# Optimization experiments

Hardware: AMD Instinct MI355X
Metric: run time of the kernel (lower is better)

## Reference

```python
import jax, jax.numpy as jnp
import numpy as np

# Static configuration (matches init_kwargs)
EMBED_DIM = 256
NUM_HEADS = 8
NUM_LEVELS = 4
NUM_POINTS = 16
N_DEGREE = 3
HEAD_DIM = EMBED_DIM // NUM_HEADS
SPATIAL_SHAPES = ((64, 64), (32, 32), (16, 16), (8, 8))  # (H, W) per level
LEN_V = sum(h * w for h, w in SPATIAL_SHAPES)


def _bilinear_gather(v, loc, Hl, Wl):
    """Bilinear sampling with zero padding, align_corners=False.
    v:   [bs, nH, Hl*Wl, hd]  flattened level feature map (per head)
    loc: [bs, nH, Q, 2]       (x, y) in [0, 1]
    returns [bs, nH, Q, hd]
    """
    x = loc[..., 0] * Wl - 0.5
    y = loc[..., 1] * Hl - 0.5
    x0 = jnp.floor(x)
    y0 = jnp.floor(y)
    wx = x - x0
    wy = y - y0
    out = jnp.zeros(v.shape[:2] + (loc.shape[2], v.shape[-1]), v.dtype)
    corners = ((0, 0, (1 - wx) * (1 - wy)), (1, 0, wx * (1 - wy)),
               (0, 1, (1 - wx) * wy), (1, 1, wx * wy))
    for dx, dy, w in corners:
        xi = x0 + dx
        yi = y0 + dy
        valid = (xi >= 0) & (xi < Wl) & (yi >= 0) & (yi < Hl)
        idx = (jnp.clip(yi, 0, Hl - 1) * Wl + jnp.clip(xi, 0, Wl - 1)).astype(jnp.int32)
        g = jnp.take_along_axis(v, idx[..., None], axis=2)  # [bs,nH,Q,hd]
        out = out + g * (w * valid.astype(w.dtype))[..., None]
    return out


def setup_inputs() -> dict:
    key = jax.random.key(0)
    ks = jax.random.split(key, 12)
    bs, Lq = 4, 1024
    s = 0.02
    return {
        "query": jax.random.normal(ks[0], (bs, Lq, EMBED_DIM), jnp.float32),
        # polynomial coefficients for x(l), y(l); scaled so curves stay roughly in [0,1]
        "reference_points": jax.random.uniform(ks[1], (bs, Lq, 2 * (N_DEGREE + 1)), jnp.float32) * 0.25,
        "value": jax.random.normal(ks[2], (bs, LEN_V, EMBED_DIM), jnp.float32),
        "W_value": jax.random.normal(ks[3], (EMBED_DIM, EMBED_DIM), jnp.float32) * s,
        "b_value": jnp.zeros((EMBED_DIM,), jnp.float32),
        "W_offsets": jax.random.normal(ks[4], (EMBED_DIM, NUM_HEADS * NUM_LEVELS * NUM_POINTS * 2), jnp.float32) * s,
        "b_offsets": jax.random.normal(ks[5], (NUM_HEADS * NUM_LEVELS * NUM_POINTS * 2,), jnp.float32) * 0.5,
        "W_attn": jax.random.normal(ks[6], (EMBED_DIM, NUM_HEADS * NUM_LEVELS * NUM_POINTS), jnp.float32) * s,
        "b_attn": jnp.zeros((NUM_HEADS * NUM_LEVELS * NUM_POINTS,), jnp.float32),
        "W_out": jax.random.normal(ks[7], (EMBED_DIM, EMBED_DIM), jnp.float32) * s,
        "b_out": jnp.zeros((EMBED_DIM,), jnp.float32),
    }


def reference(query, reference_points, value, W_value, b_value, W_offsets,
              b_offsets, W_attn, b_attn, W_out, b_out):
    bs, Lq, _ = query.shape
    Lv = value.shape[1]
    nH, nL, nP, hd = NUM_HEADS, NUM_LEVELS, NUM_POINTS, HEAD_DIM

    v = (value @ W_value + b_value).reshape(bs, Lv, nH, hd)

    sampling_offsets = (query @ W_offsets + b_offsets).reshape(bs, Lq, nH, nL, nP, 2)
    attn = jax.nn.softmax((query @ W_attn + b_attn).reshape(bs, Lq, nH, nL * nP), axis=-1)
    attn = attn.reshape(bs, Lq, nH, nL, nP)

    # reference_points last dim == 8: polynomial branch
    lambdaz = jnp.linspace(0.0, 1.0, nP)
    lambdas = jnp.stack([lambdaz ** i for i in range(N_DEGREE, -1, -1)], axis=1)  # [nP, deg+1]
    ref_polys = reference_points.reshape(bs, Lq, 2, N_DEGREE + 1)
    pnts = jnp.einsum('bqcd,pd->bqpc', ref_polys, lambdas)  # [bs,Lq,nP,2] (x,y)

    # offset_normalizer: spatial shapes flipped -> (W, H) per level
    normalizer = jnp.array([[w, h] for (h, w) in SPATIAL_SHAPES], jnp.float32)
    normalizer = normalizer.reshape(1, 1, 1, nL, 1, 2)
    sampling_locations = pnts[:, :, None, None, :, :] + sampling_offsets / normalizer
    # -> [bs, Lq, nH, nL, nP, 2] in [0,1]

    # deformable attention core: per-level bilinear gather + softmax-weighted sum
    out = jnp.zeros((bs, Lq, nH, hd), v.dtype)
    start = 0
    for lvl, (Hl, Wl) in enumerate(SPATIAL_SHAPES):
        v_l = v[:, start:start + Hl * Wl].transpose(0, 2, 1, 3)  # [bs,nH,Hl*Wl,hd]
        loc_l = sampling_locations[:, :, :, lvl]                 # [bs,Lq,nH,nP,2]
        loc_l = loc_l.transpose(0, 2, 1, 3, 4).reshape(bs, nH, Lq * nP, 2)
        sampled = _bilinear_gather(v_l, loc_l, Hl, Wl).reshape(bs, nH, Lq, nP, hd)
        out = out + jnp.einsum('bhqpd,bqhp->bqhd', sampled, attn[:, :, :, lvl])
        start += Hl * Wl

    output = out.reshape(bs, Lq, nH * hd) @ W_out + b_out
    return output, sampling_locations, attn
```

## Files before the change

### kernel.cpp

```cpp
#include <hip/hip_runtime.h>
#include <math.h>

#define BS 4
#define LQ 1024
#define EMB 256
#define NH 8
#define NL 4
#define NP 16
#define HD 32
#define LV 5440
#define KDIM 256

typedef __attribute__((ext_vector_type(8))) short short8;
typedef __attribute__((ext_vector_type(4))) float f32x4;

__device__ inline unsigned short f2bf(float f) {
    unsigned u = __builtin_bit_cast(unsigned, f);
    u += 0x7fff + ((u >> 16) & 1);
    return (unsigned short)(u >> 16);
}

__global__ __launch_bounds__(256) void prep(const float* __restrict__ Wv,
                                            const float* __restrict__ Wo,
                                            const float* __restrict__ Wa,
                                            const float* __restrict__ Wu,
                                            const float* __restrict__ value,
                                            const float* __restrict__ query,
                                            unsigned short* __restrict__ Wt,
                                            unsigned short* __restrict__ val_bf,
                                            unsigned short* __restrict__ qry_bf) {
    const int blk = blockIdx.x;
    if (blk < 512) {
        __shared__ float tile[32][33];
        const int n0 = (blk & 63) * 32, k0 = (blk >> 6) * 32;
        const float* src; int N, nloc;
        if (n0 < 256)       { src = Wv; N = 256;  nloc = n0; }
        else if (n0 < 1280) { src = Wo; N = 1024; nloc = n0 - 256; }
        else if (n0 < 1792) { src = Wa; N = 512;  nloc = n0 - 1280; }
        else                { src = Wu; N = 256;  nloc = n0 - 1792; }
        const int tx = threadIdx.x & 31, ty = threadIdx.x >> 5;
#pragma unroll
        for (int i = 0; i < 32; i += 8)
            tile[ty + i][tx] = src[(size_t)(k0 + ty + i) * N + nloc + tx];
        __syncthreads();
#pragma unroll
        for (int i = 0; i < 32; i += 8)
            Wt[(size_t)(n0 + ty + i) * KDIM + k0 + tx] = f2bf(tile[tx][ty + i]);
    } else {
        const int i = (blk - 512) * 256 + threadIdx.x;
        const float* src;
        unsigned short* dst;
        size_t off;
        if (i < 696320) { src = value; dst = val_bf; off = (size_t)i * 8; }
        else            { src = query; dst = qry_bf; off = (size_t)(i - 696320) * 8; }
        const float4 f0 = *(const float4*)(src + off);
        const float4 f1 = *(const float4*)(src + off + 4);
        short8 h;
        h[0] = (short)f2bf(f0.x); h[1] = (short)f2bf(f0.y);
        h[2] = (short)f2bf(f0.z); h[3] = (short)f2bf(f0.w);
        h[4] = (short)f2bf(f1.x); h[5] = (short)f2bf(f1.y);
        h[6] = (short)f2bf(f1.z); h[7] = (short)f2bf(f1.w);
        *(short8*)(dst + off) = h;
    }
}

template <int MODE>
__device__ __forceinline__ void gemm_nolds(const unsigned short* __restrict__ A,
                                           const unsigned short* __restrict__ Bt,
                                           const float* __restrict__ bias,
                                           const float* __restrict__ bias2,
                                           const float* __restrict__ refp,
                                           void* __restrict__ Cv,
                                           float* __restrict__ C2,
                                           int N, int bx, int by) {
    const int t = threadIdx.x;
    const int lane = t & 63, w = t >> 6;
    const int quad = lane >> 4, l16 = lane & 15;
    const int wr = w >> 1, wc = w & 1;
    const int row0 = by * 128, col0 = bx * 128;

    const unsigned short* ap = A  + (size_t)(row0 + wr * 64 + l16) * KDIM + quad * 8;
    const unsigned short* bp = Bt + (size_t)(col0 + wc * 64 + l16) * KDIM + quad * 8;

    f32x4 acc[4][4] = {};

#pragma unroll 2
    for (int kt = 0; kt < 8; ++kt) {
        short8 af[4], bf[4];
#pragma unroll
        for (int mi = 0; mi < 4; ++mi)
            af[mi] = *(const short8*)(ap + (size_t)mi * 16 * KDIM + kt * 32);
#pragma unroll
        for (int ni = 0; ni < 4; ++ni)
            bf[ni] = *(const short8*)(bp + (size_t)ni * 16 * KDIM + kt * 32);
#pragma unroll
        for (int mi = 0; mi < 4; ++mi)
#pragma unroll
            for (int ni = 0; ni < 4; ++ni)
                acc[mi][ni] = __builtin_amdgcn_mfma_f32_16x16x32_bf16(af[mi], bf[ni],
                                                                      acc[mi][ni], 0, 0, 0);
    }

    if (MODE == 0 || MODE == 2) {
#pragma unroll
        for (int ni = 0; ni < 4; ++ni) {
            const int c = col0 + wc * 64 + ni * 16 + l16;
            const float bv = bias[c];
#pragma unroll
            for (int mi = 0; mi < 4; ++mi) {
                const int r0 = row0 + wr * 64 + mi * 16 + quad * 4;
#pragma unroll
                for (int rr = 0; rr < 4; ++rr) {
                    const float o = acc[mi][ni][rr] + bv;
                    if (MODE == 0) ((float*)Cv)[(size_t)(r0 + rr) * N + c] = o;
                    else ((unsigned short*)Cv)[(size_t)(r0 + rr) * N + c] = f2bf(o);
                }
            }
        }
    } else {
        const bool is_off = (col0 < 1024);
        if (is_off) {
            float* C = (float*)Cv;
#pragma unroll
            for (int ni = 0; ni < 4; ++ni) {
                const int cg = col0 + wc * 64 + ni * 16 + l16;
                const int xy = cg & 1, p = (cg >> 1) & 15, l = (cg >> 5) & 3;
                const float lam = (float)p * (1.0f / 15.0f);
                const float l2 = lam * lam, l3 = l2 * lam;
                const float rW = (l == 0) ? 0.015625f : (l == 1) ? 0.03125f
                                : (l == 2) ? 0.0625f : 0.125f;
                const float bv = bias[cg];
#pragma unroll
                for (int mi = 0; mi < 4; ++mi) {
                    const int r0 = row0 + wr * 64 + mi * 16 + quad * 4;
#pragma unroll
                    for (int rr = 0; rr < 4; ++rr) {
                        const int r = r0 + rr;
                        const float4 rp = *(const float4*)(refp + (size_t)r * 8 + xy * 4);
                        const float poly = rp.x * l3 + rp.y * l2 + rp.z * lam + rp.w;
                        C[(size_t)r * 1024 + cg] = poly + (acc[mi][ni][rr] + bv) * rW;
                    }
                }
            }
        } else {
            const int cabase = col0 - 1024 + wc * 64;
            float bv[4];
#pragma unroll
            for (int ni = 0; ni < 4; ++ni) bv[ni] = bias2[cabase + ni * 16 + l16];
#pragma unroll
            for (int mi = 0; mi < 4; ++mi) {
                const int r0 = row0 + wr * 64 + mi * 16 + quad * 4;
#pragma unroll
                for (int rr = 0; rr < 4; ++rr) {
                    float v0 = acc[mi][0][rr] + bv[0];
                    float v1 = acc[mi][1][rr] + bv[1];
                    float v2 = acc[mi][2][rr] + bv[2];
                    float v3 = acc[mi][3][rr] + bv[3];
                    float mx = fmaxf(fmaxf(v0, v1), fmaxf(v2, v3));
#pragma unroll
                    for (int mk = 1; mk < 16; mk <<= 1) mx = fmaxf(mx, __shfl_xor(mx, mk));
                    v0 = __expf(v0 - mx); v1 = __expf(v1 - mx);
                    v2 = __expf(v2 - mx); v3 = __expf(v3 - mx);
                    float s = v0 + v1 + v2 + v3;
#pragma unroll
                    for (int mk = 1; mk < 16; mk <<= 1) s += __shfl_xor(s, mk);
                    const float inv = 1.0f / s;
                    const size_t rb = (size_t)(r0 + rr) * 512 + cabase + l16;
                    C2[rb]      = v0 * inv;
                    C2[rb + 16] = v1 * inv;
                    C2[rb + 32] = v2 * inv;
                    C2[rb + 48] = v3 * inv;
                }
            }
        }
    }
}

__global__ __launch_bounds__(256) void gemm_fused(const unsigned short* __restrict__ val_bf,
                                                  const unsigned short* __restrict__ qry_bf,
                                                  const unsigned short* __restrict__ Wt,
                                                  const float* __restrict__ b_value,
                                                  const float* __restrict__ b_off,
                                                  const float* __restrict__ b_attn,
                                                  const float* __restrict__ refp,
                                                  unsigned short* __restrict__ v_proj,
                                                  float* __restrict__ loc_out,
                                                  float* __restrict__ attn_out) {
    const int b = blockIdx.x;
    if (b < 340) {
        gemm_nolds<2>(val_bf, Wt, b_value, nullptr, nullptr,
                      v_proj, nullptr, 256, b & 1, b >> 1);
    } else {
        const int b2 = b - 340;
        gemm_nolds<1>(qry_bf, Wt + (size_t)256 * KDIM, b_off, b_attn, refp,
                      loc_out, attn_out, 1536, b2 % 12, b2 / 12);
    }
}

__global__ __launch_bounds__(256) void gemm_outp(const unsigned short* __restrict__ interm,
                                                 const unsigned short* __restrict__ Wt_out,
                                                 const float* __restrict__ b_out,
                                                 float* __restrict__ out) {
    gemm_nolds<0>(interm, Wt_out, b_out, nullptr, nullptr,
                  out, nullptr, 256, blockIdx.x & 1, blockIdx.x >> 1);
}

__global__ __launch_bounds__(256, 4) void sample_kernel(const unsigned short* __restrict__ v,
                                                        const float* __restrict__ loc,
                                                        const float* __restrict__ attn,
                                                        unsigned short* __restrict__ interm) {
    const int t = threadIdx.x;
    const int g = blockIdx.x * 16 + (t >> 4);
    const int l16i = t & 15;
    const int lvl = l16i >> 2;
    const int cq  = l16i & 3;
    const int h = g & 7, bq = g >> 3, b = bq >> 10;

    const int W = 64 >> lvl;
    const float Wf = (float)W;
    const int sh = 6 - lvl;
    const int start = (lvl == 0) ? 0 : (lvl == 1) ? 4096 : (lvl == 2) ? 5120 : 5376;

    const float* lp = loc  + (size_t)g * 128 + lvl * 32;
    const float* ap = attn + (size_t)g * 64  + lvl * 16;
    const unsigned short* vl = v + ((size_t)b * LV + start) * EMB + h * HD + cq * 8;

    float acc[8] = {};

    auto cadd = [&](const uint4 q, float wgt) {
        acc[0] = fmaf(wgt, __builtin_bit_cast(float, q.x << 16), acc[0]);
        acc[1] = fmaf(wgt, __builtin_bit_cast(float, q.x & 0xffff0000u), acc[1]);
        acc[2] = fmaf(wgt, __builtin_bit_cast(float, q.y << 16), acc[2]);
        acc[3] = fmaf(wgt, __builtin_bit_cast(float, q.y & 0xffff0000u), acc[3]);
        acc[4] = fmaf(wgt, __builtin_bit_cast(float, q.z << 16), acc[4]);
        acc[5] = fmaf(wgt, __builtin_bit_cast(float, q.z & 0xffff0000u), acc[5]);
        acc[6] = fmaf(wgt, __builtin_bit_cast(float, q.w << 16), acc[6]);
        acc[7] = fmaf(wgt, __builtin_bit_cast(float, q.w & 0xffff0000u), acc[7]);
    };

    auto point = [&](float lx, float ly, float wt) {
        const float x = lx * Wf - 0.5f, y = ly * Wf - 0.5f;
        const float x0f = floorf(x), y0f = floorf(y);
        const float wx = x - x0f, wy = y - y0f;
        const int x0 = (int)x0f, y0 = (int)y0f;
        const int x1 = x0 + 1, y1 = y0 + 1;
        const float iwx = 1.f - wx, iwy = 1.f - wy;
        float w00 = iwx * iwy * wt, w10 = wx * iwy * wt;
        float w01 = iwx * wy * wt,  w11 = wx * wy * wt;
        const bool vx0 = (unsigned)x0 < (unsigned)W;
        const bool vx1 = (unsigned)x1 < (unsigned)W;
        const bool vy0 = (unsigned)y0 < (unsigned)W;
        const bool vy1 = (unsigned)y1 < (unsigned)W;
        w00 = (vx0 & vy0) ? w00 : 0.f;
        w10 = (vx1 & vy0) ? w10 : 0.f;
        w01 = (vx0 & vy1) ? w01 : 0.f;
        w11 = (vx1 & vy1) ? w11 : 0.f;
        const int cx0 = min(max(x0, 0), W - 1);
        const int cx1 = min(max(x1, 0), W - 1);
        const int cy0 = min(max(y0, 0), W - 1);
        const int cy1 = min(max(y1, 0), W - 1);
        const uint4 g00 = *(const uint4*)(vl + (size_t)((cy0 << sh) + cx0) * EMB);
        const uint4 g10 = *(const uint4*)(vl + (size_t)((cy0 << sh) + cx1) * EMB);
        const uint4 g01 = *(const uint4*)(vl + (size_t)((cy1 << sh) + cx0) * EMB);
        const uint4 g11 = *(const uint4*)(vl + (size_t)((cy1 << sh) + cx1) * EMB);
        cadd(g00, w00); cadd(g10, w10); cadd(g01, w01); cadd(g11, w11);
    };

#pragma unroll 1
    for (int p4 = 0; p4 < 16; p4 += 4) {
        const float4 la = *(const float4*)(lp + 2 * p4);
        const float4 lb = *(const float4*)(lp + 2 * p4 + 4);
        const float4 wv = *(const float4*)(ap + p4);
        point(la.x, la.y, wv.x); point(la.z, la.w, wv.y);
        point(lb.x, lb.y, wv.z); point(lb.z, lb.w, wv.w);
    }

#pragma unroll
    for (int m = 4; m <= 8; m <<= 1)
#pragma unroll
        for (int k = 0; k < 8; ++k) acc[k] += __shfl_xor(acc[k], m);

    if (lvl == 0) {
        unsigned short o[8];
#pragma unroll
        for (int k = 0; k < 8; ++k) o[k] = f2bf(acc[k]);
        *(uint4*)(interm + (size_t)bq * EMB + h * HD + cq * 8) = *(const uint4*)o;
    }
}

extern "C" void kernel_launch(void* const* d_in, const int* in_sizes, int n_in,
                              void* d_out, int out_size, void* d_ws, size_t ws_size,
                              hipStream_t stream) {
    const float* query   = (const float*)d_in[0];
    const float* refp    = (const float*)d_in[1];
    const float* value   = (const float*)d_in[2];
    const float* W_value = (const float*)d_in[3];
    const float* b_value = (const float*)d_in[4];
    const float* W_off   = (const float*)d_in[5];
    const float* b_off   = (const float*)d_in[6];
    const float* W_attn  = (const float*)d_in[7];
    const float* b_attn  = (const float*)d_in[8];
    const float* W_out   = (const float*)d_in[9];
    const float* b_out   = (const float*)d_in[10];

    float* out      = (float*)d_out;
    float* loc_out  = out + 1048576;
    float* attn_out = out + 5242880;

    char* ws = (char*)d_ws;
    unsigned short* val_bf = (unsigned short*)ws;
    unsigned short* interm = (unsigned short*)ws;
    unsigned short* v_proj = (unsigned short*)(ws + 11141120);
    unsigned short* qry_bf = (unsigned short*)(ws + 22282240);
    unsigned short* Wt_all = (unsigned short*)(ws + 24379392);

    const dim3 blk(256);

    prep<<<3744, blk, 0, stream>>>(W_value, W_off, W_attn, W_out, value, query,
                                   Wt_all, val_bf, qry_bf);

    gemm_fused<<<724, blk, 0, stream>>>(val_bf, qry_bf, Wt_all, b_value, b_off,
                                        b_attn, refp, v_proj, loc_out, attn_out);

    sample_kernel<<<(BS * LQ * NH) / 16, blk, 0, stream>>>(v_proj, loc_out, attn_out, interm);

    gemm_outp<<<64, blk, 0, stream>>>(interm, Wt_all + (size_t)1792 * KDIM, b_out, out);
}
```

Baseline: 183.4 us.

## Pre-tile GEMM operands for MFMA and zero-pad value maps to drop bounds checks

The prep kernel now writes weights, value and query in an MFMA fragment-tiled layout, so each lane's GEMM loads become contiguous 512-element strides. The value projection is written into a zero-bordered padded layout per level, letting the sampler drop the validity masks and per-corner clamping in favour of one clamp and fixed neighbour offsets. Bilinear accumulation uses packed float2 math, and launch_bounds min-blocks of 2 is added to the GEMMs. This adds a border-zeroing pass and a scattered bf16 epilogue for the value projection, and clamping to the padded border must reproduce the zero-padding semantics exactly.

```diff
diff --git a/kernel.cpp b/kernel.cpp
--- a/kernel.cpp
+++ b/kernel.cpp
@@ -9,6 +9,7 @@
 #define NP 16
 #define HD 32
 #define LV 5440
+#define LVP 5936
 #define KDIM 256
 
 typedef __attribute__((ext_vector_type(8))) short short8;
@@ -19,6 +20,7 @@
     u += 0x7fff + ((u >> 16) & 1);
     return (unsigned short)(u >> 16);
 }
+
 
 __global__ __launch_bounds__(256) void prep(const float* __restrict__ Wv,
                                             const float* __restrict__ Wo,
@@ -28,8 +30,10 @@
                                             const float* __restrict__ query,
                                             unsigned short* __restrict__ Wt,
                                             unsigned short* __restrict__ val_bf,
-                                            unsigned short* __restrict__ qry_bf) {
+                                            unsigned short* __restrict__ qry_bf,
+                                            unsigned short* __restrict__ v_pad) {
     const int blk = blockIdx.x;
+    const int t = threadIdx.x;
     if (blk < 512) {
         __shared__ float tile[32][33];
         const int n0 = (blk & 63) * 32, k0 = (blk >> 6) * 32;
@@ -38,29 +42,53 @@
         else if (n0 < 1280) { src = Wo; N = 1024; nloc = n0 - 256; }
         else if (n0 < 1792) { src = Wa; N = 512;  nloc = n0 - 1280; }
         else                { src = Wu; N = 256;  nloc = n0 - 1792; }
-        const int tx = threadIdx.x & 31, ty = threadIdx.x >> 5;
+        const int tx = t & 31, ty = t >> 5;
 #pragma unroll
         for (int i = 0; i < 32; i += 8)
             tile[ty + i][tx] = src[(size_t)(k0 + ty + i) * N + nloc + tx];
         __syncthreads();
-#pragma unroll
-        for (int i = 0; i < 32; i += 8)
-            Wt[(size_t)(n0 + ty + i) * KDIM + k0 + tx] = f2bf(tile[tx][ty + i]);
-    } else {
-        const int i = (blk - 512) * 256 + threadIdx.x;
-        const float* src;
-        unsigned short* dst;
-        size_t off;
-        if (i < 696320) { src = value; dst = val_bf; off = (size_t)i * 8; }
-        else            { src = query; dst = qry_bf; off = (size_t)(i - 696320) * 8; }
-        const float4 f0 = *(const float4*)(src + off);
-        const float4 f1 = *(const float4*)(src + off + 4);
+        if (t < 128) {
+            const int n_loc = t & 31, oct = t >> 5;
+            const int n = n0 + n_loc;
+            short8 h;
+#pragma unroll
+            for (int e = 0; e < 8; ++e) h[e] = (short)f2bf(tile[oct * 8 + e][n_loc]);
+            const size_t off = ((size_t)(n >> 4) * 8 + (k0 >> 5)) * 512
+                             + ((n & 15) + 16 * oct) * 8;
+            *(short8*)(Wt + off) = h;
+        }
+    } else if (blk < 3744) {
+        int i; const float* src; unsigned short* dst;
+        if (blk < 3232) { i = (blk - 512) * 256 + t;  src = value; dst = val_bf; }
+        else            { i = (blk - 3232) * 256 + t; src = query; dst = qry_bf; }
+        const int r = i >> 5, oct = i & 31, k0 = oct * 8;
+        const float4 f0 = *(const float4*)(src + (size_t)r * KDIM + k0);
+        const float4 f1 = *(const float4*)(src + (size_t)r * KDIM + k0 + 4);
         short8 h;
         h[0] = (short)f2bf(f0.x); h[1] = (short)f2bf(f0.y);
         h[2] = (short)f2bf(f0.z); h[3] = (short)f2bf(f0.w);
         h[4] = (short)f2bf(f1.x); h[5] = (short)f2bf(f1.y);
         h[6] = (short)f2bf(f1.z); h[7] = (short)f2bf(f1.w);
+        const size_t off = ((size_t)(r >> 4) * 8 + (oct >> 2)) * 512
+                         + ((r & 15) + 16 * (oct & 3)) * 8;
         *(short8*)(dst + off) = h;
+    } else {
+        const int pidx = (blk - 3744) * 8 + (t >> 5);
+        const int lane32 = t & 31;
+        const unsigned b = (unsigned)pidx / 496u;
+        const unsigned rem = (unsigned)pidx - b * 496u;
+        int Wd, W2, pb, i;
+        if (rem < 260)      { Wd = 64; W2 = 66; pb = 0;    i = rem; }
+        else if (rem < 392) { Wd = 32; W2 = 34; pb = 4356; i = rem - 260; }
+        else if (rem < 460) { Wd = 16; W2 = 18; pb = 5512; i = rem - 392; }
+        else                { Wd = 8;  W2 = 10; pb = 5836; i = rem - 460; }
+        int y, x;
+        if (i < W2)          { y = 0;      x = i; }
+        else if (i < 2 * W2) { y = Wd + 1; x = i - W2; }
+        else { const int j = i - 2 * W2; y = 1 + (j >> 1); x = (j & 1) ? (Wd + 1) : 0; }
+        const size_t off = ((size_t)b * LVP + pb + y * W2 + x) * EMB + lane32 * 8;
+        uint4 z = {0, 0, 0, 0};
+        *(uint4*)(v_pad + off) = z;
     }
 }
 
@@ -79,8 +107,8 @@
     const int wr = w >> 1, wc = w & 1;
     const int row0 = by * 128, col0 = bx * 128;
 
-    const unsigned short* ap = A  + (size_t)(row0 + wr * 64 + l16) * KDIM + quad * 8;
-    const unsigned short* bp = Bt + (size_t)(col0 + wc * 64 + l16) * KDIM + quad * 8;
+    const unsigned short* ap = A  + ((size_t)((row0 >> 4) + wr * 4) * 8) * 512 + lane * 8;
+    const unsigned short* bp = Bt + ((size_t)((col0 >> 4) + wc * 4) * 8) * 512 + lane * 8;
 
     f32x4 acc[4][4] = {};
 
@@ -89,10 +117,10 @@
         short8 af[4], bf[4];
 #pragma unroll
         for (int mi = 0; mi < 4; ++mi)
-            af[mi] = *(const short8*)(ap + (size_t)mi * 16 * KDIM + kt * 32);
+            af[mi] = *(const short8*)(ap + (size_t)mi * 4096 + kt * 512);
 #pragma unroll
         for (int ni = 0; ni < 4; ++ni)
-            bf[ni] = *(const short8*)(bp + (size_t)ni * 16 * KDIM + kt * 32);
+            bf[ni] = *(const short8*)(bp + (size_t)ni * 4096 + kt * 512);
 #pragma unroll
         for (int mi = 0; mi < 4; ++mi)
 #pragma unroll
@@ -101,7 +129,7 @@
                                                                       acc[mi][ni], 0, 0, 0);
     }
 
-    if (MODE == 0 || MODE == 2) {
+    if (MODE == 0) {
 #pragma unroll
         for (int ni = 0; ni < 4; ++ni) {
             const int c = col0 + wc * 64 + ni * 16 + l16;
@@ -110,11 +138,35 @@
             for (int mi = 0; mi < 4; ++mi) {
                 const int r0 = row0 + wr * 64 + mi * 16 + quad * 4;
 #pragma unroll
-                for (int rr = 0; rr < 4; ++rr) {
-                    const float o = acc[mi][ni][rr] + bv;
-                    if (MODE == 0) ((float*)Cv)[(size_t)(r0 + rr) * N + c] = o;
-                    else ((unsigned short*)Cv)[(size_t)(r0 + rr) * N + c] = f2bf(o);
-                }
+                for (int rr = 0; rr < 4; ++rr)
+                    ((float*)Cv)[(size_t)(r0 + rr) * N + c] = acc[mi][ni][rr] + bv;
+            }
+        }
+    } else if (MODE == 2) {
+        unsigned short* C = (unsigned short*)Cv;
+        float bv[4];
+        int cc[4];
+#pragma unroll
+        for (int ni = 0; ni < 4; ++ni) {
+            cc[ni] = col0 + wc * 64 + ni * 16 + l16;
+            bv[ni] = bias[cc[ni]];
+        }
+#pragma unroll
+        for (int mi = 0; mi < 4; ++mi) {
+#pragma unroll
+            for (int rr = 0; rr < 4; ++rr) {
+                const unsigned r = row0 + wr * 64 + mi * 16 + quad * 4 + rr;
+                const unsigned b = r / 5440u;
+                const unsigned flat = r - b * 5440u;
+                unsigned y, x, W2, pb;
+                if (flat < 4096)      { y = flat >> 6; x = flat & 63; W2 = 66; pb = 0; }
+                else if (flat < 5120) { const unsigned f = flat - 4096; y = f >> 5; x = f & 31; W2 = 34; pb = 4356; }
+                else if (flat < 5376) { const unsigned f = flat - 5120; y = f >> 4; x = f & 15; W2 = 18; pb = 5512; }
+                else                  { const unsigned f = flat - 5376; y = f >> 3; x = f & 7;  W2 = 10; pb = 5836; }
+                const size_t rowbase = ((size_t)b * LVP + pb + (y + 1) * W2 + (x + 1)) * EMB;
+#pragma unroll
+                for (int ni = 0; ni < 4; ++ni)
+                    C[rowbase + cc[ni]] = f2bf(acc[mi][ni][rr] + bv[ni]);
             }
         }
     } else {
@@ -176,20 +228,20 @@
     }
 }
 
-__global__ __launch_bounds__(256) void gemm_fused(const unsigned short* __restrict__ val_bf,
-                                                  const unsigned short* __restrict__ qry_bf,
-                                                  const unsigned short* __restrict__ Wt,
-                                                  const float* __restrict__ b_value,
-                                                  const float* __restrict__ b_off,
-                                                  const float* __restrict__ b_attn,
-                                                  const float* __restrict__ refp,
-                                                  unsigned short* __restrict__ v_proj,
-                                                  float* __restrict__ loc_out,
-                                                  float* __restrict__ attn_out) {
+__global__ __launch_bounds__(256, 2) void gemm_fused(const unsigned short* __restrict__ val_bf,
+                                                     const unsigned short* __restrict__ qry_bf,
+                                                     const unsigned short* __restrict__ Wt,
+                                                     const float* __restrict__ b_value,
+                                                     const float* __restrict__ b_off,
+                                                     const float* __restrict__ b_attn,
+                                                     const float* __restrict__ refp,
+                                                     unsigned short* __restrict__ v_pad,
+                                                     float* __restrict__ loc_out,
+                                                     float* __restrict__ attn_out) {
     const int b = blockIdx.x;
     if (b < 340) {
         gemm_nolds<2>(val_bf, Wt, b_value, nullptr, nullptr,
-                      v_proj, nullptr, 256, b & 1, b >> 1);
+                      v_pad, nullptr, 256, b & 1, b >> 1);
     } else {
         const int b2 = b - 340;
         gemm_nolds<1>(qry_bf, Wt + (size_t)256 * KDIM, b_off, b_attn, refp,
@@ -197,10 +249,10 @@
     }
 }
 
-__global__ __launch_bounds__(256) void gemm_outp(const unsigned short* __restrict__ interm,
-                                                 const unsigned short* __restrict__ Wt_out,
-                                                 const float* __restrict__ b_out,
-                                                 float* __restrict__ out) {
+__global__ __launch_bounds__(256, 2) void gemm_outp(const unsigned short* __restrict__ interm,
+                                                    const unsigned short* __restrict__ Wt_out,
+                                                    const float* __restrict__ b_out,
+                                                    float* __restrict__ out) {
     gemm_nolds<0>(interm, Wt_out, b_out, nullptr, nullptr,
                   out, nullptr, 256, blockIdx.x & 1, blockIdx.x >> 1);
 }
@@ -216,53 +268,48 @@
     const int cq  = l16i & 3;
     const int h = g & 7, bq = g >> 3, b = bq >> 10;
 
-    const int W = 64 >> lvl;
-    const float Wf = (float)W;
-    const int sh = 6 - lvl;
-    const int start = (lvl == 0) ? 0 : (lvl == 1) ? 4096 : (lvl == 2) ? 5120 : 5376;
+    const int Wd = 64 >> lvl;
+    const float Wf = (float)Wd;
+    const int W2 = Wd + 2;
+    const int rowoff = W2 * EMB;
+    const int pb = (lvl == 0) ? 0 : (lvl == 1) ? 4356 : (lvl == 2) ? 5512 : 5836;
 
     const float* lp = loc  + (size_t)g * 128 + lvl * 32;
     const float* ap = attn + (size_t)g * 64  + lvl * 16;
-    const unsigned short* vl = v + ((size_t)b * LV + start) * EMB + h * HD + cq * 8;
-
-    float acc[8] = {};
-
+    const unsigned short* vl = v + ((size_t)b * LVP + pb) * EMB + h * HD + cq * 8;
+
+    float2 acc2[4] = {};
+
+    auto cvt2 = [](unsigned d) {
+        uint2 u; u.x = d << 16; u.y = d & 0xffff0000u;
+        return __builtin_bit_cast(float2, u);
+    };
     auto cadd = [&](const uint4 q, float wgt) {
-        acc[0] = fmaf(wgt, __builtin_bit_cast(float, q.x << 16), acc[0]);
-        acc[1] = fmaf(wgt, __builtin_bit_cast(float, q.x & 0xffff0000u), acc[1]);
-        acc[2] = fmaf(wgt, __builtin_bit_cast(float, q.y << 16), acc[2]);
-        acc[3] = fmaf(wgt, __builtin_bit_cast(float, q.y & 0xffff0000u), acc[3]);
-        acc[4] = fmaf(wgt, __builtin_bit_cast(float, q.z << 16), acc[4]);
-        acc[5] = fmaf(wgt, __builtin_bit_cast(float, q.z & 0xffff0000u), acc[5]);
-        acc[6] = fmaf(wgt, __builtin_bit_cast(float, q.w << 16), acc[6]);
-        acc[7] = fmaf(wgt, __builtin_bit_cast(float, q.w & 0xffff0000u), acc[7]);
+        const float2 w2 = make_float2(wgt, wgt);
+        acc2[0] += cvt2(q.x) * w2;
+        acc2[1] += cvt2(q.y) * w2;
+        acc2[2] += cvt2(q.z) * w2;
+        acc2[3] += cvt2(q.w) * w2;
     };
 
     auto point = [&](float lx, float ly, float wt) {
-        const float x = lx * Wf - 0.5f, y = ly * Wf - 0.5f;
-        const float x0f = floorf(x), y0f = floorf(y);
-        const float wx = x - x0f, wy = y - y0f;
-        const int x0 = (int)x0f, y0 = (int)y0f;
-        const int x1 = x0 + 1, y1 = y0 + 1;
-        const float iwx = 1.f - wx, iwy = 1.f - wy;
-        float w00 = iwx * iwy * wt, w10 = wx * iwy * wt;
-        float w01 = iwx * wy * wt,  w11 = wx * wy * wt;
-        const bool vx0 = (unsigned)x0 < (unsigned)W;
-        const bool vx1 = (unsigned)x1 < (unsigned)W;
-        const bool vy0 = (unsigned)y0 < (unsigned)W;
-        const bool vy1 = (unsigned)y1 < (unsigned)W;
-        w00 = (vx0 & vy0) ? w00 : 0.f;
-        w10 = (vx1 & vy0) ? w10 : 0.f;
-        w01 = (vx0 & vy1) ? w01 : 0.f;
-        w11 = (vx1 & vy1) ? w11 : 0.f;
-        const int cx0 = min(max(x0, 0), W - 1);
-        const int cx1 = min(max(x1, 0), W - 1);
-        const int cy0 = min(max(y0, 0), W - 1);
-        const int cy1 = min(max(y1, 0), W - 1);
-        const uint4 g00 = *(const uint4*)(vl + (size_t)((cy0 << sh) + cx0) * EMB);
-        const uint4 g10 = *(const uint4*)(vl + (size_t)((cy0 << sh) + cx1) * EMB);
-        const uint4 g01 = *(const uint4*)(vl + (size_t)((cy1 << sh) + cx0) * EMB);
-        const uint4 g11 = *(const uint4*)(vl + (size_t)((cy1 << sh) + cx1) * EMB);
+        const float x = fmaf(lx, Wf, -0.5f);
+        const float y = fmaf(ly, Wf, -0.5f);
+        const float xc = fminf(fmaxf(x, -1.0f), Wf);
+        const float yc = fminf(fmaxf(y, -1.0f), Wf);
+        const float x0f = fminf(floorf(xc), Wf - 1.0f);
+        const float y0f = fminf(floorf(yc), Wf - 1.0f);
+        const float wx = xc - x0f, wy = yc - y0f;
+        const float iwx = 1.0f - wx, iwy = 1.0f - wy;
+        const int px = (int)x0f + 1;
+        const int py = (int)y0f + 1;
+        const int base = (py * W2 + px) * EMB;
+        const float w00 = iwx * iwy * wt, w10 = wx * iwy * wt;
+        const float w01 = iwx * wy * wt,  w11 = wx * wy * wt;
+        const uint4 g00 = *(const uint4*)(vl + base);
+        const uint4 g10 = *(const uint4*)(vl + base + EMB);
+        const uint4 g01 = *(const uint4*)(vl + base + rowoff);
+        const uint4 g11 = *(const uint4*)(vl + base + rowoff + EMB);
         cadd(g00, w00); cadd(g10, w10); cadd(g01, w01); cadd(g11, w11);
     };
 
@@ -275,16 +322,20 @@
         point(lb.x, lb.y, wv.z); point(lb.z, lb.w, wv.w);
     }
 
+    float a[8] = {acc2[0].x, acc2[0].y, acc2[1].x, acc2[1].y,
+                  acc2[2].x, acc2[2].y, acc2[3].x, acc2[3].y};
 #pragma unroll
     for (int m = 4; m <= 8; m <<= 1)
 #pragma unroll
-        for (int k = 0; k < 8; ++k) acc[k] += __shfl_xor(acc[k], m);
+        for (int k = 0; k < 8; ++k) a[k] += __shfl_xor(a[k], m);
 
     if (lvl == 0) {
         unsigned short o[8];
 #pragma unroll
-        for (int k = 0; k < 8; ++k) o[k] = f2bf(acc[k]);
-        *(uint4*)(interm + (size_t)bq * EMB + h * HD + cq * 8) = *(const uint4*)o;
+        for (int k = 0; k < 8; ++k) o[k] = f2bf(a[k]);
+        const size_t off = ((size_t)(bq >> 4) * 8 + h) * 512
+                         + ((bq & 15) + 16 * cq) * 8;
+        *(uint4*)(interm + off) = *(const uint4*)o;
     }
 }
 
@@ -308,21 +359,21 @@
     float* attn_out = out + 5242880;
 
     char* ws = (char*)d_ws;
-    unsigned short* val_bf = (unsigned short*)ws;
-    unsigned short* interm = (unsigned short*)ws;
-    unsigned short* v_proj = (unsigned short*)(ws + 11141120);
-    unsigned short* qry_bf = (unsigned short*)(ws + 22282240);
-    unsigned short* Wt_all = (unsigned short*)(ws + 24379392);
+    unsigned short* v_pad  = (unsigned short*)ws;
+    unsigned short* val_bf = (unsigned short*)(ws + 12156928);
+    unsigned short* interm = (unsigned short*)(ws + 12156928);
+    unsigned short* qry_bf = (unsigned short*)(ws + 23298048);
+    unsigned short* Wt_all = (unsigned short*)(ws + 25395200);
 
     const dim3 blk(256);
 
-    prep<<<3744, blk, 0, stream>>>(W_value, W_off, W_attn, W_out, value, query,
-                                   Wt_all, val_bf, qry_bf);
+    prep<<<3992, blk, 0, stream>>>(W_value, W_off, W_attn, W_out, value, query,
+                                   Wt_all, val_bf, qry_bf, v_pad);
 
     gemm_fused<<<724, blk, 0, stream>>>(val_bf, qry_bf, Wt_all, b_value, b_off,
-                                        b_attn, refp, v_proj, loc_out, attn_out);
-
-    sample_kernel<<<(BS * LQ * NH) / 16, blk, 0, stream>>>(v_proj, loc_out, attn_out, interm);
+                                        b_attn, refp, v_pad, loc_out, attn_out);
+
+    sample_kernel<<<(BS * LQ * NH) / 16, blk, 0, stream>>>(v_pad, loc_out, attn_out, interm);
 
     gemm_outp<<<64, blk, 0, stream>>>(interm, Wt_all + (size_t)1792 * KDIM, b_out, out);
 }
```

Measured after the change: 165.6 us. 9.7% less time.
